# Optimization experiments

Measured on AMD Instinct MI355X. Metric: run time of the kernel, lower is better.

Reference implementation:

```python
import jax, jax.numpy as jnp
import numpy as np
import math

H = 8
D_MODEL = 512
SEQ = 1024  # afr_reduced_cnn_size -> becomes sequence/channel axis
B = 16
KSIZE = 7
D_K = D_MODEL // H


def setup_inputs() -> dict:
    key = jax.random.key(0)
    ks = jax.random.split(key, 9)
    s = 0.02
    return {
        "query": jax.random.normal(ks[0], (B, SEQ, D_MODEL), jnp.float32),
        "key": jax.random.normal(ks[1], (B, SEQ, D_MODEL), jnp.float32),
        "value": jax.random.normal(ks[2], (B, SEQ, D_MODEL), jnp.float32),
        # causal conv params for K and V projections (convs[1], convs[2]); convs[0] is unused in forward
        "conv_k_w": jax.random.normal(ks[3], (SEQ, SEQ, KSIZE), jnp.float32) * s,
        "conv_k_b": jnp.zeros((SEQ,), jnp.float32),
        "conv_v_w": jax.random.normal(ks[4], (SEQ, SEQ, KSIZE), jnp.float32) * s,
        "conv_v_b": jnp.zeros((SEQ,), jnp.float32),
        # output linear (torch Linear: weight [out, in])
        "lin_w": jax.random.normal(ks[5], (D_MODEL, D_MODEL), jnp.float32) * s,
        "lin_b": jnp.zeros((D_MODEL,), jnp.float32),
    }


def _causal_conv1d(x, w, b):
    # x: [B, C, L]; w: [O, I, K]; left-pad K-1 for causality
    pad = w.shape[-1] - 1
    y = jax.lax.conv_general_dilated(
        x, w, window_strides=(1,), padding=[(pad, 0)],
        dimension_numbers=("NCH", "OIH", "NCH"))
    return y + b[None, :, None]


def reference(query, key, value, conv_k_w, conv_k_b, conv_v_w, conv_v_b, lin_w, lin_b):
    nb = query.shape[0]
    # [B, S, d_model] -> [B, h, N, d_k]
    q = query.reshape(nb, -1, H, D_K).transpose(0, 2, 1, 3)
    k = _causal_conv1d(key, conv_k_w, conv_k_b).reshape(nb, -1, H, D_K).transpose(0, 2, 1, 3)
    v = _causal_conv1d(value, conv_v_w, conv_v_b).reshape(nb, -1, H, D_K).transpose(0, 2, 1, 3)
    scores = jnp.einsum("bhnd,bhmd->bhnm", q, k) / math.sqrt(D_K)
    p_attn = jax.nn.softmax(scores, axis=-1)  # dropout is identity at eval
    x = jnp.einsum("bhnm,bhmd->bhnd", p_attn, v)
    x = x.transpose(0, 2, 1, 3).reshape(nb, -1, H * D_K)
    return x @ lin_w.T + lin_b
```

## Files before the change

### kernel.cpp

```cpp
#include <hip/hip_runtime.h>
#include <hip/hip_bf16.h>

typedef unsigned short u16;
typedef __attribute__((ext_vector_type(8))) __bf16 bf16x8;
typedef __attribute__((ext_vector_type(4))) float f32x4;
typedef __attribute__((ext_vector_type(4))) unsigned short u16x4;

#define DEVI static __device__ __forceinline__

DEVI u16 f2bf(float f) {
    union { float f; unsigned u; } v; v.f = f;
    unsigned r = v.u + 0x7fffu + ((v.u >> 16) & 1u);
    return (u16)(r >> 16);
}

DEVI unsigned cvt_pk_bf16(float lo, float hi) {
    unsigned r;
    asm("v_cvt_pk_bf16_f32 %0, %1, %2" : "=v"(r) : "v"(lo), "v"(hi));
    return r;
}

DEVI void gload16(const u16* g, u16* l) {
    __builtin_amdgcn_global_load_lds(
        (const __attribute__((address_space(1))) void*)g,
        (__attribute__((address_space(3))) void*)l, 16, 0, 0);
}


__global__ void k_cast_scale(const float* __restrict__ src, u16* __restrict__ dst,
                             int n, float scale) {
    int i = (blockIdx.x * blockDim.x + threadIdx.x) * 4;
    if (i >= n) return;
    float4 v = *(const float4*)(src + i);
    u16x4 o = { f2bf(v.x * scale), f2bf(v.y * scale), f2bf(v.z * scale), f2bf(v.w * scale) };
    *(u16x4*)(dst + i) = o;
}

__global__ void k_castW(const float* __restrict__ w, u16* __restrict__ wt) {
    int oi = blockIdx.x * blockDim.x + threadIdx.x;
    const float* p = w + (size_t)oi * 7;
#pragma unroll
    for (int t = 0; t < 7; ++t)
        wt[(size_t)t * 1048576 + oi] = f2bf(p[t]);
}

__global__ void k_transpose_pad(const float* __restrict__ x, u16* __restrict__ out) {
    __shared__ float tile[64][65];
    int b = blockIdx.z;
    int l0 = blockIdx.x * 64, i0 = blockIdx.y * 64;
    int t = threadIdx.x;
    const float* xb = x + (size_t)b * 1024 * 512;
    u16* ob = out + (size_t)b * 520 * 1024;
    int tr = t >> 4, tc = (t & 15) * 4;
#pragma unroll
    for (int r = 0; r < 4; ++r) {
        int row = tr + r * 16;
        float4 v = *(const float4*)(xb + (size_t)(i0 + row) * 512 + l0 + tc);
        tile[row][tc + 0] = v.x; tile[row][tc + 1] = v.y;
        tile[row][tc + 2] = v.z; tile[row][tc + 3] = v.w;
    }
    __syncthreads();
#pragma unroll
    for (int r = 0; r < 4; ++r) {
        int lr = tr + r * 16;
        u16x4 o = { f2bf(tile[tc + 0][lr]), f2bf(tile[tc + 1][lr]),
                    f2bf(tile[tc + 2][lr]), f2bf(tile[tc + 3][lr]) };
        *(u16x4*)(ob + (size_t)(l0 + 6 + lr) * 1024 + i0 + tc) = o;
    }
}

__global__ __launch_bounds__(512, 2)
void k_conv256(const u16* __restrict__ WtK, const u16* __restrict__ WtV,
               const u16* __restrict__ XtK, const u16* __restrict__ XtV,
               const float* __restrict__ bK, const float* __restrict__ bV,
               u16* __restrict__ YK, u16* __restrict__ YV) {
    __shared__ __align__(16) u16 As[2][16384];
    __shared__ __align__(16) u16 Bs[2][16384];
    int z = blockIdx.z;
    bool isV = z >= 16;
    int b = isV ? z - 16 : z;
    const u16* Wt = isV ? WtV : WtK;
    const u16* Xb = (isV ? XtV : XtK) + (size_t)b * 520 * 1024;
    int o0 = blockIdx.y * 256, l0 = blockIdx.x * 256;
    int tid = threadIdx.x, lane = tid & 63, wave = tid >> 6;
    int q = lane & 15, g = lane >> 4;
    int wm = wave >> 2, wn = wave & 3;

    int sr = tid >> 3;
    int ss = (tid & 7) ^ (sr & 7);

    auto stage = [&](int j, int slot) {
        int t = j >> 4, i0 = (j & 15) << 6;
        const u16* a  = Wt + ((size_t)t << 20) + (size_t)(o0 + sr) * 1024 + i0 + ss * 8;
        const u16* bb = Xb + (size_t)(l0 + t + sr) * 1024 + i0 + ss * 8;
        u16* ad = &As[slot][tid * 8];
        u16* bd = &Bs[slot][tid * 8];
#pragma unroll
        for (int l = 0; l < 4; ++l) {
            gload16(a  + (size_t)(l << 6) * 1024, ad + (l << 12));
            gload16(bb + (size_t)(l << 6) * 1024, bd + (l << 12));
        }
    };

    f32x4 acc[8][4] = {};

    stage(0, 0);
    stage(1, 1);
    asm volatile("s_waitcnt vmcnt(8)" ::: "memory");
    __builtin_amdgcn_s_barrier();

    for (int j = 0; j < 112; ++j) {
        int slot = j & 1;
        const u16* Asl = As[slot];
        const u16* Bsl = Bs[slot];
        bf16x8 bfr[4][2], af[4][2];
#pragma unroll
        for (int nf = 0; nf < 4; ++nf) {
            int r = wn * 64 + nf * 16 + q;
            const u16* base = Bsl + r * 64;
#pragma unroll
            for (int kk = 0; kk < 2; ++kk)
                bfr[nf][kk] = *(const bf16x8*)(base + (((kk * 4 + g) ^ (r & 7)) << 3));
        }
#pragma unroll
        for (int mf = 0; mf < 4; ++mf) {
            int r = wm * 128 + mf * 16 + q;
            const u16* base = Asl + r * 64;
#pragma unroll
            for (int kk = 0; kk < 2; ++kk)
                af[mf][kk] = *(const bf16x8*)(base + (((kk * 4 + g) ^ (r & 7)) << 3));
        }
        __builtin_amdgcn_s_setprio(1);
#pragma unroll
        for (int mf = 0; mf < 4; ++mf)
#pragma unroll
            for (int nf = 0; nf < 4; ++nf)
#pragma unroll
                for (int kk = 0; kk < 2; ++kk)
                    acc[mf][nf] = __builtin_amdgcn_mfma_f32_16x16x32_bf16(af[mf][kk], bfr[nf][kk], acc[mf][nf], 0, 0, 0);
        __builtin_amdgcn_s_setprio(0);
#pragma unroll
        for (int mf = 0; mf < 4; ++mf) {
            int r = wm * 128 + 64 + mf * 16 + q;
            const u16* base = Asl + r * 64;
#pragma unroll
            for (int kk = 0; kk < 2; ++kk)
                af[mf][kk] = *(const bf16x8*)(base + (((kk * 4 + g) ^ (r & 7)) << 3));
        }
        __builtin_amdgcn_s_setprio(1);
#pragma unroll
        for (int mf = 0; mf < 4; ++mf)
#pragma unroll
            for (int nf = 0; nf < 4; ++nf)
#pragma unroll
                for (int kk = 0; kk < 2; ++kk)
                    acc[4 + mf][nf] = __builtin_amdgcn_mfma_f32_16x16x32_bf16(af[mf][kk], bfr[nf][kk], acc[4 + mf][nf], 0, 0, 0);
        __builtin_amdgcn_s_setprio(0);

        asm volatile("" ::: "memory");
        __builtin_amdgcn_s_barrier();
        if (j + 2 < 112) {
            stage(j + 2, slot);
            asm volatile("s_waitcnt vmcnt(8)" ::: "memory");
        } else {
            asm volatile("s_waitcnt vmcnt(0)" ::: "memory");
        }
        __builtin_amdgcn_s_barrier();
        asm volatile("" ::: "memory");
    }

    const float* bias = isV ? bV : bK;
#pragma unroll
    for (int mf = 0; mf < 8; ++mf) {
        int ro = o0 + wm * 128 + mf * 16 + g * 4;
        float b0 = bias[ro + 0], b1 = bias[ro + 1], b2 = bias[ro + 2], b3 = bias[ro + 3];
#pragma unroll
        for (int nf = 0; nf < 4; ++nf) {
            int co = l0 + wn * 64 + nf * 16 + q;
            f32x4 a = acc[mf][nf];
            if (isV) {
                u16x4 o = { f2bf(a[0] + b0), f2bf(a[1] + b1), f2bf(a[2] + b2), f2bf(a[3] + b3) };
                *(u16x4*)&YV[((size_t)b * 512 + co) * 1024 + ro] = o;
            } else {
                u16* yp = &YK[((size_t)b * 1024 + ro) * 512 + co];
                yp[0]    = f2bf(a[0] + b0);
                yp[512]  = f2bf(a[1] + b1);
                yp[1024] = f2bf(a[2] + b2);
                yp[1536] = f2bf(a[3] + b3);
            }
        }
    }
}

__global__ __launch_bounds__(512, 4)
void k_attn2(const u16* __restrict__ Q, const u16* __restrict__ K,
             const u16* __restrict__ Vt, u16* __restrict__ O) {
    __shared__ __align__(16) u16 Ks[2][64 * 64];
    __shared__ __align__(16) u16 Vs[2][64 * 64];
    int b = blockIdx.z, h = blockIdx.y, q0 = blockIdx.x * 128;
    int tid = threadIdx.x, lane = tid & 63, wave = tid >> 6;
    int g = lane >> 4, q = lane & 15;

    const u16* Kb = K + (size_t)b * 1024 * 512 + h * 64;
    const u16* Vb = Vt + ((size_t)b * 512 + h * 64) * 1024;
    const u16* Qb = Q + ((size_t)b * 1024 + q0 + wave * 16 + q) * 512 + h * 64;

    bf16x8 qf[2];
    qf[0] = *(const bf16x8*)(Qb + g * 8);
    qf[1] = *(const bf16x8*)(Qb + 32 + g * 8);

    int sr = tid >> 3;
    int ss = (tid & 7) ^ (sr & 7);
    const u16* ksrc = Kb + (size_t)sr * 512 + ss * 8;
    const u16* vsrc = Vb + (size_t)sr * 1024 + ss * 8;

    f32x4 o[4] = {};
    float lsum = 0.f;

    gload16(ksrc, &Ks[0][tid * 8]);
    gload16(vsrc, &Vs[0][tid * 8]);
    __syncthreads();

#pragma unroll 2
    for (int t = 0; t < 16; ++t) {
        int buf = t & 1;
        if (t < 15) {
            gload16(ksrc + (size_t)(t + 1) * 64 * 512, &Ks[buf ^ 1][tid * 8]);
            gload16(vsrc + (t + 1) * 64, &Vs[buf ^ 1][tid * 8]);
        }
        f32x4 s[4];
#pragma unroll
        for (int mf = 0; mf < 4; ++mf) {
            int r = 16 * mf + q;
            const u16* base = &Ks[buf][r * 64];
            bf16x8 kf0 = *(const bf16x8*)(base + (((g) ^ (q & 7)) << 3));
            bf16x8 kf1 = *(const bf16x8*)(base + (((4 + g) ^ (q & 7)) << 3));
            f32x4 zz = {};
            zz = __builtin_amdgcn_mfma_f32_16x16x32_bf16(kf0, qf[0], zz, 0, 0, 0);
            s[mf] = __builtin_amdgcn_mfma_f32_16x16x32_bf16(kf1, qf[1], zz, 0, 0, 0);
        }
        unsigned w[4][2];
#pragma unroll
        for (int mf = 0; mf < 4; ++mf) {
            f32x4 p;
#pragma unroll
            for (int j = 0; j < 4; ++j) {
                p[j] = exp2f(s[mf][j]);
                lsum += p[j];
            }
            w[mf][0] = cvt_pk_bf16(p[0], p[1]);
            w[mf][1] = cvt_pk_bf16(p[2], p[3]);
        }
        bool hi = lane >= 32;
        int ia = ((g & 1) << 5) + q;
        int ib = ia + 16;
#pragma unroll
        for (int c = 0; c < 2; ++c) {
            unsigned a0 = __shfl(w[2 * c][0], ia), b0 = __shfl(w[2 * c + 1][0], ia);
            unsigned a1 = __shfl(w[2 * c][1], ia), b1 = __shfl(w[2 * c + 1][1], ia);
            unsigned a2 = __shfl(w[2 * c][0], ib), b2 = __shfl(w[2 * c + 1][0], ib);
            unsigned a3 = __shfl(w[2 * c][1], ib), b3 = __shfl(w[2 * c + 1][1], ib);
            union { unsigned u[4]; bf16x8 v8; } pu;
            pu.u[0] = hi ? b0 : a0;
            pu.u[1] = hi ? b1 : a1;
            pu.u[2] = hi ? b2 : a2;
            pu.u[3] = hi ? b3 : a3;
            bf16x8 pb = pu.v8;
#pragma unroll
            for (int df = 0; df < 4; ++df) {
                int rd = 16 * df + q;
                bf16x8 vf = *(const bf16x8*)(&Vs[buf][rd * 64] + (((c * 4 + g) ^ (q & 7)) << 3));
                o[df] = __builtin_amdgcn_mfma_f32_16x16x32_bf16(vf, pb, o[df], 0, 0, 0);
            }
        }
        __syncthreads();
    }

    lsum += __shfl_xor(lsum, 16);
    lsum += __shfl_xor(lsum, 32);
    float inv = 1.0f / lsum;

    unsigned wo[4][2];
#pragma unroll
    for (int df = 0; df < 4; ++df) {
        f32x4 v = o[df];
        v[0] *= inv; v[1] *= inv; v[2] *= inv; v[3] *= inv;
        wo[df][0] = cvt_pk_bf16(v[0], v[1]);
        wo[df][1] = cvt_pk_bf16(v[2], v[3]);
    }
    bool hi = lane >= 32;
    int ia = ((g & 1) << 5) + q;
    int ib = ia + 16;
    u16* Ob = O + ((size_t)b * 1024 + q0 + wave * 16 + q) * 512 + h * 64;
#pragma unroll
    for (int c = 0; c < 2; ++c) {
        unsigned a0 = __shfl(wo[2 * c][0], ia), b0 = __shfl(wo[2 * c + 1][0], ia);
        unsigned a1 = __shfl(wo[2 * c][1], ia), b1 = __shfl(wo[2 * c + 1][1], ia);
        unsigned a2 = __shfl(wo[2 * c][0], ib), b2 = __shfl(wo[2 * c + 1][0], ib);
        unsigned a3 = __shfl(wo[2 * c][1], ib), b3 = __shfl(wo[2 * c + 1][1], ib);
        int4 st;
        st.x = (int)(hi ? b0 : a0);
        st.y = (int)(hi ? b1 : a1);
        st.z = (int)(hi ? b2 : a2);
        st.w = (int)(hi ? b3 : a3);
        *(int4*)(Ob + c * 32 + g * 8) = st;
    }
}

__global__ __launch_bounds__(256, 2)
void k_gemm_out(const u16* __restrict__ A, const u16* __restrict__ Bt,
                const float* __restrict__ bias, float* __restrict__ C) {
    __shared__ __align__(16) u16 As[128 * 64];
    __shared__ __align__(16) u16 Bs[128 * 64];
    int n0 = blockIdx.x * 128, m0 = blockIdx.y * 128;
    int tid = threadIdx.x, lane = tid & 63, wave = tid >> 6;
    int wr = (wave >> 1) * 64, wc = (wave & 1) * 64;
    f32x4 acc[4][4] = {};

    for (int kk = 0; kk < 8; ++kk) {
        int i0 = kk * 64;
        const u16* asrc = A + (size_t)(m0 + (tid >> 3)) * 512 + i0 + (tid & 7) * 8;
        const u16* bsrc = Bt + (size_t)(n0 + (tid >> 3)) * 512 + i0 + (tid & 7) * 8;
        __syncthreads();
#pragma unroll
        for (int s = 0; s < 4; ++s) {
            gload16(asrc + (size_t)s * 32 * 512, &As[s * 2048 + tid * 8]);
            gload16(bsrc + (size_t)s * 32 * 512, &Bs[s * 2048 + tid * 8]);
        }
        __syncthreads();
#pragma unroll
        for (int ks = 0; ks < 2; ++ks) {
            bf16x8 af[4], bfr[4];
#pragma unroll
            for (int m = 0; m < 4; ++m)
                af[m] = *(const bf16x8*)&As[(wr + m * 16 + (lane & 15)) * 64 + ks * 32 + (lane >> 4) * 8];
#pragma unroll
            for (int n = 0; n < 4; ++n)
                bfr[n] = *(const bf16x8*)&Bs[(wc + n * 16 + (lane & 15)) * 64 + ks * 32 + (lane >> 4) * 8];
#pragma unroll
            for (int m = 0; m < 4; ++m)
#pragma unroll
                for (int n = 0; n < 4; ++n)
                    acc[m][n] = __builtin_amdgcn_mfma_f32_16x16x32_bf16(af[m], bfr[n], acc[m][n], 0, 0, 0);
        }
    }

#pragma unroll
    for (int m = 0; m < 4; ++m) {
        int ro = m0 + wr + m * 16 + (lane >> 4) * 4;
#pragma unroll
        for (int n = 0; n < 4; ++n) {
            int co = n0 + wc + n * 16 + (lane & 15);
            float bb = bias[co];
            float* cp = &C[(size_t)ro * 512 + co];
            cp[0]    = acc[m][n][0] + bb;
            cp[512]  = acc[m][n][1] + bb;
            cp[1024] = acc[m][n][2] + bb;
            cp[1536] = acc[m][n][3] + bb;
        }
    }
}

extern "C" void kernel_launch(void* const* d_in, const int* in_sizes, int n_in,
                              void* d_out, int out_size, void* d_ws, size_t ws_size,
                              hipStream_t stream) {
    (void)in_sizes; (void)n_in; (void)out_size; (void)ws_size;
    const float* query = (const float*)d_in[0];
    const float* key   = (const float*)d_in[1];
    const float* value = (const float*)d_in[2];
    const float* wk    = (const float*)d_in[3];
    const float* bk    = (const float*)d_in[4];
    const float* wv    = (const float*)d_in[5];
    const float* bv    = (const float*)d_in[6];
    const float* lw    = (const float*)d_in[7];
    const float* lb    = (const float*)d_in[8];
    float* out = (float*)d_out;

    u16* ws16  = (u16*)d_ws;
    u16* q_bf  = ws16;
    u16* k_att = q_bf  + 8388608;
    u16* v_t   = k_att + 8388608;
    u16* x_att = v_t   + 8388608;
    u16* xt_k  = x_att + 8388608;
    u16* xt_v  = xt_k  + 8519680;
    u16* wk_bf = xt_v  + 8519680;
    u16* wv_bf = wk_bf + 7340032;
    u16* lw_bf = wv_bf + 7340032;

    hipMemsetAsync(xt_k, 0, (size_t)2 * 8519680 * sizeof(u16), stream);

    k_cast_scale<<<8192, 256, 0, stream>>>(query, q_bf, 8388608, 0.125f * 1.44269504f);
    k_cast_scale<<<256, 256, 0, stream>>>(lw, lw_bf, 262144, 1.0f);
    k_castW<<<4096, 256, 0, stream>>>(wk, wk_bf);
    k_castW<<<4096, 256, 0, stream>>>(wv, wv_bf);
    k_transpose_pad<<<dim3(8, 16, 16), 256, 0, stream>>>(key, xt_k);
    k_transpose_pad<<<dim3(8, 16, 16), 256, 0, stream>>>(value, xt_v);

    k_conv256<<<dim3(2, 4, 32), 512, 0, stream>>>(wk_bf, wv_bf, xt_k, xt_v, bk, bv, k_att, v_t);

    k_attn2<<<dim3(8, 8, 16), 512, 0, stream>>>(q_bf, k_att, v_t, x_att);

    k_gemm_out<<<dim3(4, 128), 256, 0, stream>>>(x_att, lw_bf, lb, out);
}
```

Measured before the change: 364.5 us.

## Remap conv blocks to XCDs for weight L2 reuse and interleave A-fragment loads with MFMA

The conv GEMM grid becomes 1D and each block id is decoded so that blocks on the same XCD (id & 7) share one K/V weight tile (o0, isV). The aim is to keep the weight slice in that XCD's L2 across batches. The inner loop now loads A fragments in four smaller groups, each followed by an MFMA burst wrapped in barriers. This lowers register pressure and interleaves LDS reads with MFMA work, but it adds more barriers per iteration.

Result: slower. 394.1 us (+8.1%).

```diff
diff --git a/kernel.cpp b/kernel.cpp
--- a/kernel.cpp
+++ b/kernel.cpp
@@ -76,12 +76,14 @@
                u16* __restrict__ YK, u16* __restrict__ YV) {
     __shared__ __align__(16) u16 As[2][16384];
     __shared__ __align__(16) u16 Bs[2][16384];
-    int z = blockIdx.z;
-    bool isV = z >= 16;
-    int b = isV ? z - 16 : z;
+    int id = blockIdx.x;
+    int xcd = id & 7, inner = id >> 3;
+    bool isV = xcd & 1;
+    int o0 = (xcd >> 1) * 256;
+    int b = inner & 15;
+    int l0 = (inner >> 4) * 256;
     const u16* Wt = isV ? WtV : WtK;
     const u16* Xb = (isV ? XtV : XtK) + (size_t)b * 520 * 1024;
-    int o0 = blockIdx.y * 256, l0 = blockIdx.x * 256;
     int tid = threadIdx.x, lane = tid & 63, wave = tid >> 6;
     int q = lane & 15, g = lane >> 4;
     int wm = wave >> 2, wn = wave & 3;
@@ -113,7 +115,7 @@
         int slot = j & 1;
         const u16* Asl = As[slot];
         const u16* Bsl = Bs[slot];
-        bf16x8 bfr[4][2], af[4][2];
+        bf16x8 bfr[4][2];
 #pragma unroll
         for (int nf = 0; nf < 4; ++nf) {
             int r = wn * 64 + nf * 16 + q;
@@ -123,42 +125,29 @@
                 bfr[nf][kk] = *(const bf16x8*)(base + (((kk * 4 + g) ^ (r & 7)) << 3));
         }
 #pragma unroll
-        for (int mf = 0; mf < 4; ++mf) {
-            int r = wm * 128 + mf * 16 + q;
-            const u16* base = Asl + r * 64;
-#pragma unroll
-            for (int kk = 0; kk < 2; ++kk)
-                af[mf][kk] = *(const bf16x8*)(base + (((kk * 4 + g) ^ (r & 7)) << 3));
-        }
-        __builtin_amdgcn_s_setprio(1);
-#pragma unroll
-        for (int mf = 0; mf < 4; ++mf)
-#pragma unroll
-            for (int nf = 0; nf < 4; ++nf)
+        for (int p = 0; p < 4; ++p) {
+            bf16x8 af[2][2];
+#pragma unroll
+            for (int m2 = 0; m2 < 2; ++m2) {
+                int r = wm * 128 + (2 * p + m2) * 16 + q;
+                const u16* base = Asl + r * 64;
 #pragma unroll
                 for (int kk = 0; kk < 2; ++kk)
-                    acc[mf][nf] = __builtin_amdgcn_mfma_f32_16x16x32_bf16(af[mf][kk], bfr[nf][kk], acc[mf][nf], 0, 0, 0);
-        __builtin_amdgcn_s_setprio(0);
-#pragma unroll
-        for (int mf = 0; mf < 4; ++mf) {
-            int r = wm * 128 + 64 + mf * 16 + q;
-            const u16* base = Asl + r * 64;
-#pragma unroll
-            for (int kk = 0; kk < 2; ++kk)
-                af[mf][kk] = *(const bf16x8*)(base + (((kk * 4 + g) ^ (r & 7)) << 3));
-        }
-        __builtin_amdgcn_s_setprio(1);
-#pragma unroll
-        for (int mf = 0; mf < 4; ++mf)
-#pragma unroll
-            for (int nf = 0; nf < 4; ++nf)
-#pragma unroll
-                for (int kk = 0; kk < 2; ++kk)
-                    acc[4 + mf][nf] = __builtin_amdgcn_mfma_f32_16x16x32_bf16(af[mf][kk], bfr[nf][kk], acc[4 + mf][nf], 0, 0, 0);
-        __builtin_amdgcn_s_setprio(0);
-
-        asm volatile("" ::: "memory");
-        __builtin_amdgcn_s_barrier();
+                    af[m2][kk] = *(const bf16x8*)(base + (((kk * 4 + g) ^ (r & 7)) << 3));
+            }
+            __builtin_amdgcn_s_barrier();
+            __builtin_amdgcn_s_setprio(1);
+#pragma unroll
+            for (int m2 = 0; m2 < 2; ++m2)
+#pragma unroll
+                for (int nf = 0; nf < 4; ++nf)
+#pragma unroll
+                    for (int kk = 0; kk < 2; ++kk)
+                        acc[2 * p + m2][nf] = __builtin_amdgcn_mfma_f32_16x16x32_bf16(
+                            af[m2][kk], bfr[nf][kk], acc[2 * p + m2][nf], 0, 0, 0);
+            __builtin_amdgcn_s_setprio(0);
+            __builtin_amdgcn_s_barrier();
+        }
         if (j + 2 < 112) {
             stage(j + 2, slot);
             asm volatile("s_waitcnt vmcnt(8)" ::: "memory");
@@ -166,7 +155,6 @@
             asm volatile("s_waitcnt vmcnt(0)" ::: "memory");
         }
         __builtin_amdgcn_s_barrier();
-        asm volatile("" ::: "memory");
     }
 
     const float* bias = isV ? bV : bK;
@@ -396,7 +384,7 @@
     k_transpose_pad<<<dim3(8, 16, 16), 256, 0, stream>>>(key, xt_k);
     k_transpose_pad<<<dim3(8, 16, 16), 256, 0, stream>>>(value, xt_v);
 
-    k_conv256<<<dim3(2, 4, 32), 512, 0, stream>>>(wk_bf, wv_bf, xt_k, xt_v, bk, bv, k_att, v_t);
+    k_conv256<<<dim3(256, 1, 1), 512, 0, stream>>>(wk_bf, wv_bf, xt_k, xt_v, bk, bv, k_att, v_t);
 
     k_attn2<<<dim3(8, 8, 16), 512, 0, stream>>>(q_bf, k_att, v_t, x_att);
 
```

## Reuse staged input tile across all seven conv taps and remap blocks to XCDs

Applied to the files above, without the earlier changes.

The causal conv GEMM now loads each 64-channel input slab once, with 263 rows (256 plus a 7-row halo), and reuses it for all 7 kernel taps by offsetting the LDS row index, instead of reloading the shifted input for every tap. Only the weight tiles are restaged per tap, which cuts global and LDS fill traffic for the B operand by about sevenfold. The grid is flattened to 1D and remapped so that blocks sharing the same weight rows (same K/V and output block) land on the same XCD, which should improve L2 reuse of weights. Costs are a slightly larger LDS footprint and more complex wait-count bookkeeping, and the shifted row reads may break the XOR swizzle alignment and cause bank conflicts.

After: 338.9 us. 7.0% less time.

```diff
diff --git a/kernel.cpp b/kernel.cpp
--- a/kernel.cpp
+++ b/kernel.cpp
@@ -75,13 +75,15 @@
                const float* __restrict__ bK, const float* __restrict__ bV,
                u16* __restrict__ YK, u16* __restrict__ YV) {
     __shared__ __align__(16) u16 As[2][16384];
-    __shared__ __align__(16) u16 Bs[2][16384];
-    int z = blockIdx.z;
-    bool isV = z >= 16;
-    int b = isV ? z - 16 : z;
+    __shared__ __align__(16) u16 Bs[2][16896];
+    int id = blockIdx.x;
+    int xcd = id & 7, inner = id >> 3;
+    bool isV = xcd & 1;
+    int o0 = (xcd >> 1) * 256;
+    int b = inner & 15;
+    int l0 = (inner >> 4) * 256;
     const u16* Wt = isV ? WtV : WtK;
     const u16* Xb = (isV ? XtV : XtK) + (size_t)b * 520 * 1024;
-    int o0 = blockIdx.y * 256, l0 = blockIdx.x * 256;
     int tid = threadIdx.x, lane = tid & 63, wave = tid >> 6;
     int q = lane & 15, g = lane >> 4;
     int wm = wave >> 2, wn = wave & 3;
@@ -89,84 +91,101 @@
     int sr = tid >> 3;
     int ss = (tid & 7) ^ (sr & 7);
 
-    auto stage = [&](int j, int slot) {
-        int t = j >> 4, i0 = (j & 15) << 6;
-        const u16* a  = Wt + ((size_t)t << 20) + (size_t)(o0 + sr) * 1024 + i0 + ss * 8;
-        const u16* bb = Xb + (size_t)(l0 + t + sr) * 1024 + i0 + ss * 8;
+    auto stageA = [&](int ic, int t, int slot) {
+        const u16* a = Wt + ((size_t)t << 20) + (size_t)(o0 + sr) * 1024 + (ic << 6) + ss * 8;
         u16* ad = &As[slot][tid * 8];
+#pragma unroll
+        for (int l = 0; l < 4; ++l)
+            gload16(a + (size_t)(l << 6) * 1024, ad + (l << 12));
+    };
+    auto stageB = [&](int ic, int slot) {
+        const u16* bb = Xb + (size_t)(l0 + sr) * 1024 + (ic << 6) + ss * 8;
         u16* bd = &Bs[slot][tid * 8];
 #pragma unroll
-        for (int l = 0; l < 4; ++l) {
-            gload16(a  + (size_t)(l << 6) * 1024, ad + (l << 12));
+        for (int l = 0; l < 4; ++l)
             gload16(bb + (size_t)(l << 6) * 1024, bd + (l << 12));
-        }
+        int sr5 = 256 + ((tid >> 3) & 7);
+        gload16(Xb + (size_t)(l0 + sr5) * 1024 + (ic << 6) + ss * 8,
+                &Bs[slot][sr5 * 64 + (tid & 7) * 8]);
     };
 
     f32x4 acc[8][4] = {};
 
-    stage(0, 0);
-    stage(1, 1);
-    asm volatile("s_waitcnt vmcnt(8)" ::: "memory");
+    stageB(0, 0);
+    stageA(0, 0, 0);
+    stageA(0, 1, 1);
+    asm volatile("s_waitcnt vmcnt(4)" ::: "memory");
     __builtin_amdgcn_s_barrier();
 
-    for (int j = 0; j < 112; ++j) {
-        int slot = j & 1;
-        const u16* Asl = As[slot];
-        const u16* Bsl = Bs[slot];
-        bf16x8 bfr[4][2], af[4][2];
-#pragma unroll
-        for (int nf = 0; nf < 4; ++nf) {
-            int r = wn * 64 + nf * 16 + q;
-            const u16* base = Bsl + r * 64;
-#pragma unroll
-            for (int kk = 0; kk < 2; ++kk)
-                bfr[nf][kk] = *(const bf16x8*)(base + (((kk * 4 + g) ^ (r & 7)) << 3));
-        }
-#pragma unroll
-        for (int mf = 0; mf < 4; ++mf) {
-            int r = wm * 128 + mf * 16 + q;
-            const u16* base = Asl + r * 64;
-#pragma unroll
-            for (int kk = 0; kk < 2; ++kk)
-                af[mf][kk] = *(const bf16x8*)(base + (((kk * 4 + g) ^ (r & 7)) << 3));
-        }
-        __builtin_amdgcn_s_setprio(1);
-#pragma unroll
-        for (int mf = 0; mf < 4; ++mf)
-#pragma unroll
-            for (int nf = 0; nf < 4; ++nf)
+    int ic2 = 0, t2 = 2;
+    for (int ic = 0; ic < 16; ++ic) {
+        int bslot = ic & 1;
+        const u16* Bsl = Bs[bslot];
+        for (int t = 0; t < 7; ++t) {
+            int s = ic * 7 + t;
+            const u16* Asl = As[s & 1];
+            bf16x8 bfr[4][2], af[4][2];
+#pragma unroll
+            for (int nf = 0; nf < 4; ++nf) {
+                int r = wn * 64 + nf * 16 + q + t;
+                const u16* base = Bsl + r * 64;
 #pragma unroll
                 for (int kk = 0; kk < 2; ++kk)
-                    acc[mf][nf] = __builtin_amdgcn_mfma_f32_16x16x32_bf16(af[mf][kk], bfr[nf][kk], acc[mf][nf], 0, 0, 0);
-        __builtin_amdgcn_s_setprio(0);
-#pragma unroll
-        for (int mf = 0; mf < 4; ++mf) {
-            int r = wm * 128 + 64 + mf * 16 + q;
-            const u16* base = Asl + r * 64;
-#pragma unroll
-            for (int kk = 0; kk < 2; ++kk)
-                af[mf][kk] = *(const bf16x8*)(base + (((kk * 4 + g) ^ (r & 7)) << 3));
-        }
-        __builtin_amdgcn_s_setprio(1);
-#pragma unroll
-        for (int mf = 0; mf < 4; ++mf)
-#pragma unroll
-            for (int nf = 0; nf < 4; ++nf)
+                    bfr[nf][kk] = *(const bf16x8*)(base + (((kk * 4 + g) ^ (r & 7)) << 3));
+            }
+#pragma unroll
+            for (int mf = 0; mf < 4; ++mf) {
+                int r = wm * 128 + mf * 16 + q;
+                const u16* base = Asl + r * 64;
 #pragma unroll
                 for (int kk = 0; kk < 2; ++kk)
-                    acc[4 + mf][nf] = __builtin_amdgcn_mfma_f32_16x16x32_bf16(af[mf][kk], bfr[nf][kk], acc[4 + mf][nf], 0, 0, 0);
-        __builtin_amdgcn_s_setprio(0);
-
-        asm volatile("" ::: "memory");
-        __builtin_amdgcn_s_barrier();
-        if (j + 2 < 112) {
-            stage(j + 2, slot);
-            asm volatile("s_waitcnt vmcnt(8)" ::: "memory");
-        } else {
-            asm volatile("s_waitcnt vmcnt(0)" ::: "memory");
-        }
-        __builtin_amdgcn_s_barrier();
-        asm volatile("" ::: "memory");
+                    af[mf][kk] = *(const bf16x8*)(base + (((kk * 4 + g) ^ (r & 7)) << 3));
+            }
+            __builtin_amdgcn_s_setprio(1);
+#pragma unroll
+            for (int mf = 0; mf < 4; ++mf)
+#pragma unroll
+                for (int nf = 0; nf < 4; ++nf)
+#pragma unroll
+                    for (int kk = 0; kk < 2; ++kk)
+                        acc[mf][nf] = __builtin_amdgcn_mfma_f32_16x16x32_bf16(
+                            af[mf][kk], bfr[nf][kk], acc[mf][nf], 0, 0, 0);
+            __builtin_amdgcn_s_setprio(0);
+#pragma unroll
+            for (int mf = 0; mf < 4; ++mf) {
+                int r = wm * 128 + 64 + mf * 16 + q;
+                const u16* base = Asl + r * 64;
+#pragma unroll
+                for (int kk = 0; kk < 2; ++kk)
+                    af[mf][kk] = *(const bf16x8*)(base + (((kk * 4 + g) ^ (r & 7)) << 3));
+            }
+            __builtin_amdgcn_s_setprio(1);
+#pragma unroll
+            for (int mf = 0; mf < 4; ++mf)
+#pragma unroll
+                for (int nf = 0; nf < 4; ++nf)
+#pragma unroll
+                    for (int kk = 0; kk < 2; ++kk)
+                        acc[4 + mf][nf] = __builtin_amdgcn_mfma_f32_16x16x32_bf16(
+                            af[mf][kk], bfr[nf][kk], acc[4 + mf][nf], 0, 0, 0);
+            __builtin_amdgcn_s_setprio(0);
+
+            asm volatile("" ::: "memory");
+            __builtin_amdgcn_s_barrier();
+            bool haveB = (t == 2) && (ic < 15);
+            if (s + 2 < 112) {
+                stageA(ic2, t2, s & 1);
+                if (++t2 == 7) { t2 = 0; ++ic2; }
+                if (haveB) stageB(ic + 1, bslot ^ 1);
+                if (haveB || (t == 3 && ic < 15))
+                    asm volatile("s_waitcnt vmcnt(9)" ::: "memory");
+                else
+                    asm volatile("s_waitcnt vmcnt(4)" ::: "memory");
+            } else {
+                asm volatile("s_waitcnt vmcnt(0)" ::: "memory");
+            }
+            __builtin_amdgcn_s_barrier();
+        }
     }
 
     const float* bias = isV ? bV : bK;
@@ -396,7 +415,7 @@
     k_transpose_pad<<<dim3(8, 16, 16), 256, 0, stream>>>(key, xt_k);
     k_transpose_pad<<<dim3(8, 16, 16), 256, 0, stream>>>(value, xt_v);
 
-    k_conv256<<<dim3(2, 4, 32), 512, 0, stream>>>(wk_bf, wv_bf, xt_k, xt_v, bk, bv, k_att, v_t);
+    k_conv256<<<dim3(256, 1, 1), 512, 0, stream>>>(wk_bf, wv_bf, xt_k, xt_v, bk, bv, k_att, v_t);
 
     k_attn2<<<dim3(8, 8, 16), 512, 0, stream>>>(q_bf, k_att, v_t, x_att);
 
```
